# Kernel tuning notes

Measured on AMD Instinct MI355X. Metric: run time of the kernel, lower is better.

Reference implementation:

```python
import jax, jax.numpy as jnp
import numpy as np

B = 64          # graphs in batch
NPG = 9         # nodes per graph (max_atoms = NUM_ATOMS = 9)
N = B * NPG     # total nodes = 576
H = 128         # node_dim == hid_dim
SPEC_LEN = 1801
SPEC_COMP = 100
BOND = 3
ASL = BOND * 9 * 9  # action_space_length = 243


def _linear_init(key, fan_in, fan_out):
    # torch.nn.Linear default init: U(-1/sqrt(fan_in), 1/sqrt(fan_in)); stored as [in, out]
    kw, kb = jax.random.split(key)
    bound = 1.0 / np.sqrt(fan_in)
    W = jax.random.uniform(kw, (fan_in, fan_out), jnp.float32, -bound, bound)
    b = jax.random.uniform(kb, (fan_out,), jnp.float32, -bound, bound)
    return W, b


def setup_inputs() -> dict:
    key = jax.random.key(0)
    ks = jax.random.split(key, 10)
    node_features = jax.random.normal(ks[0], (N, H), jnp.float32)
    specs = jax.random.normal(ks[1], (B, 1, SPEC_LEN), jnp.float32)
    # len_vec[b, i] = 1 iff node i belongs to graph b (contiguous 9-node blocks)
    gid = np.repeat(np.arange(B), NPG)
    len_vec = jnp.asarray((gid[None, :] == np.arange(B)[:, None]).astype(np.float32))
    mask = jnp.zeros((B, ASL), jnp.float32)  # additive action mask (0 = allowed)
    indexmask = jax.random.randint(ks[2], (B, ASL), 0, ASL, dtype=jnp.int32)
    W1, b1 = _linear_init(ks[3], SPEC_LEN, SPEC_LEN // 2)
    W2, b2 = _linear_init(ks[4], SPEC_LEN // 2, SPEC_COMP)
    Wv1, bv1 = _linear_init(ks[5], H + SPEC_COMP, H // 2)
    Wv2, bv2 = _linear_init(ks[6], H // 2, 1)
    Wa2, ba2 = _linear_init(ks[7], 2 * H + SPEC_COMP, H)
    Wf, bf = _linear_init(ks[8], H, BOND)
    return {"node_features": node_features, "specs": specs, "len_vec": len_vec,
            "mask": mask, "indexmask": indexmask,
            "W1": W1, "b1": b1, "W2": W2, "b2": b2,
            "Wv1": Wv1, "bv1": bv1, "Wv2": Wv2, "bv2": bv2,
            "Wa2": Wa2, "ba2": ba2, "Wf": Wf, "bf": bf}


def reference(node_features, specs, len_vec, mask, indexmask,
              W1, b1, W2, b2, Wv1, bv1, Wv2, bv2, Wa2, ba2, Wf, bf):
    relu = jax.nn.relu
    n_total, hdim = node_features.shape
    bsz = specs.shape[0]
    npg = n_total // bsz

    # --- spectrum compression: [B,1801] -> [B,100] ---
    s = relu(specs[:, 0, :] @ W1 + b1)
    s = relu(s @ W2 + b2)

    # --- value head: SumPooling readout + spec -> scalar per graph ---
    readout = node_features.reshape(bsz, npg, hdim).sum(axis=1)
    v = relu(jnp.concatenate([readout, s], axis=-1) @ Wv1 + bv1) @ Wv2 + bv2  # [B,1]

    # --- pairwise action features ---
    # original: apf[i,j] = relu(cat(nf[i], nf[j], canvas[i,j])) then Linear(action_2).
    # relu is elementwise and Linear splits over the concat, so factorize:
    #   apf @ Wa2 = relu(nf)[i] @ Wa2[:H]  +  relu(nf)[j] @ Wa2[H:2H]  +  relu(canvas)[i,j] @ Wa2[2H:]
    # canvas is the block-diagonal scatter of s (s >= 0 so relu(canvas) = canvas).
    gid = jnp.arange(n_total) // npg
    same = gid[:, None] == gid[None, :]          # block-diagonal [N,N]
    nf_r = relu(node_features)
    Ai = nf_r @ Wa2[:hdim]                        # [N,H] per-row (Y2) term
    Bj = nf_r @ Wa2[hdim:2 * hdim]                # [N,H] per-col (X2) term
    D = s @ Wa2[2 * hdim:]                        # [B,H] spec-canvas term
    h = relu(Ai[:, None, :] + Bj[None, :, :]
             + jnp.where(same[:, :, None], D[gid][:, None, :], 0.0) + ba2)  # [N,N,H]

    len_matrix = (len_vec.T @ len_vec)[:, :, None]  # block-diagonal pair mask [N,N,1]
    saf = (h @ Wf + bf) * len_matrix                # [N,N,BOND]

    # --- per-graph action assembly (replaces nonzero()+pad+index_select loop) ---
    # with npg nodes per graph the nonzeros of saf are exactly the diagonal
    # npg x npg blocks, flattened (i, j, bond)-major, npg*npg*BOND == ASL.
    rows = jnp.arange(bsz)[:, None] * npg + jnp.arange(npg)[None, :]   # [B,npg]
    fp = saf[rows[:, :, None], rows[:, None, :], :].reshape(bsz, npg * npg * saf.shape[-1])
    gathered = jnp.take_along_axis(fp, indexmask.astype(jnp.int32), axis=1)
    return jax.nn.softmax(gathered + mask, axis=1), v
```

## Files before the change

### kernel.cpp

```cpp
#include <hip/hip_runtime.h>
#include <math.h>

#define BATCH 64
#define NPG 9
#define N_NODES 576
#define HD 128
#define SPEC_LEN 1801
#define S1DIM 900
#define SCOMP 100
#define ASL 243
#define NT 15
#define KC 17
#define KCH 106
#define KPAD 112
#define KT 1856

__global__ __launch_bounds__(256) void k_prep(const float* __restrict__ specs,
                                              const float* __restrict__ nf,
                                              const float* __restrict__ Wa2,
                                              float* __restrict__ sT,
                                              float* __restrict__ zbase,
                                              float* __restrict__ AB) {
    int bb = blockIdx.x, tid = threadIdx.x;
    if (bb < 29) {
        __shared__ float t[64 * 65];
        int k0 = bb * 64;
        int kk = tid & 63, mq = tid >> 6;
#pragma unroll
        for (int p = 0; p < 16; ++p) {
            int m = p * 4 + mq;
            int k = k0 + kk;
            float v = (k < SPEC_LEN) ? specs[(size_t)m * SPEC_LEN + k] : 0.0f;
            t[kk * 65 + m] = v;
        }
        __syncthreads();
#pragma unroll
        for (int p = 0; p < 16; ++p) {
            int o = p * 256 + tid;
            sT[(size_t)k0 * 64 + o] = t[(o >> 6) * 65 + (o & 63)];
        }
    } else if (bb < 92) {
        int idx = (bb - 29) * 1024 + tid * 4;
        if (idx < BATCH * S1DIM + BATCH * SCOMP)
            *(float4*)(zbase + idx) = make_float4(0.f, 0.f, 0.f, 0.f);
    } else {
        __shared__ float snf[4 * HD];
        int ib = (bb - 92) * 4;
        snf[tid]       = fmaxf(nf[(size_t)ib * HD + tid], 0.0f);
        snf[256 + tid] = fmaxf(nf[(size_t)ib * HD + 256 + tid], 0.0f);
        __syncthreads();
        int c = tid;
        const float* __restrict__ wp = (c < HD) ? (Wa2 + c) : (Wa2 + HD * HD + (c - HD));
        float a0 = 0.f, a1 = 0.f, a2 = 0.f, a3 = 0.f;
#pragma unroll 16
        for (int k = 0; k < HD; ++k) {
            float w = wp[(size_t)k * HD];
            a0 = fmaf(snf[k], w, a0);
            a1 = fmaf(snf[HD + k], w, a1);
            a2 = fmaf(snf[2 * HD + k], w, a2);
            a3 = fmaf(snf[3 * HD + k], w, a3);
        }
        AB[(size_t)(ib + 0) * 256 + c] = a0;
        AB[(size_t)(ib + 1) * 256 + c] = a1;
        AB[(size_t)(ib + 2) * 256 + c] = a2;
        AB[(size_t)(ib + 3) * 256 + c] = a3;
    }
}

__global__ __launch_bounds__(256) void k_gemm1(const float* __restrict__ sT,
                                               const float* __restrict__ W1,
                                               float* __restrict__ s1pre) {
    __shared__ float w1t[KPAD][64];
    int bb = blockIdx.x, tid = threadIdx.x;
    int nt = bb % NT, kc = bb / NT;
    int n0 = nt * 64;
    int kb = kc * KCH;
    int klen = min(KCH, SPEC_LEN - kb);
    int lane = tid & 63;
    int m0 = __builtin_amdgcn_readfirstlane(tid >> 6) * 16;

#pragma unroll 7
    for (int e = tid; e < KPAD * 64; e += 256) {
        int kl = e >> 6, nn = e & 63;
        float v = 0.0f;
        if (kl < klen && (n0 + nn) < S1DIM)
            v = W1[(size_t)(kb + kl) * S1DIM + n0 + nn];
        w1t[kl][nn] = v;
    }
    __syncthreads();

    float acc[16];
#pragma unroll
    for (int i = 0; i < 16; ++i) acc[i] = 0.0f;

    const float* __restrict__ sp = sT + (size_t)kb * 64 + m0;
#pragma unroll 4
    for (int kk = 0; kk < KPAD; ++kk) {
        float w = w1t[kk][lane];
        const float* __restrict__ sa = sp + kk * 64;
#pragma unroll
        for (int i = 0; i < 16; ++i)
            acc[i] = fmaf(sa[i], w, acc[i]);
    }

    int n = n0 + lane;
    if (n < S1DIM) {
#pragma unroll
        for (int i = 0; i < 16; ++i)
            atomicAdd(&s1pre[(size_t)(m0 + i) * S1DIM + n], acc[i]);
    }
}

__global__ __launch_bounds__(128) void k_gemm2(const float* __restrict__ s1pre,
                                               const float* __restrict__ b1,
                                               const float* __restrict__ W2,
                                               float* __restrict__ s1c) {
    __shared__ float sld[SCOMP];
    int bb = blockIdx.x, tid = threadIdx.x;
    int m = bb / 9;
    int kb = (bb % 9) * 100;
    if (tid < 100)
        sld[tid] = fmaxf(s1pre[(size_t)m * S1DIM + kb + tid] + b1[kb + tid], 0.0f);
    __syncthreads();
    if (tid < SCOMP) {
        float a = 0.0f;
#pragma unroll 10
        for (int kl = 0; kl < 100; ++kl)
            a = fmaf(sld[kl], W2[(size_t)(kb + kl) * SCOMP + tid], a);
        atomicAdd(&s1c[(size_t)m * SCOMP + tid], a);
    }
}

__global__ __launch_bounds__(256) void k_head(const float* __restrict__ s1c,
                                              const float* __restrict__ b2,
                                              const float* __restrict__ Wa2,
                                              const float* __restrict__ nf,
                                              const float* __restrict__ Wv1,
                                              const float* __restrict__ bv1,
                                              const float* __restrict__ Wv2,
                                              const float* __restrict__ bv2,
                                              const float* __restrict__ ba2,
                                              const float* __restrict__ Wf,
                                              const float* __restrict__ bfb,
                                              const int* __restrict__ indexmask,
                                              const float* __restrict__ mask,
                                              const float* __restrict__ AB,
                                              float* __restrict__ out,
                                              float* __restrict__ vout) {
    int m = blockIdx.x, tid = threadIdx.x;
    __shared__ __align__(16) float sAi[NPG * 132];
    __shared__ __align__(16) float sBj[NPG * 132];
    __shared__ __align__(16) float sWfT[3 * 132];
    __shared__ __align__(16) float srow[SCOMP];
    __shared__ __align__(16) float ro[HD];
    __shared__ __align__(16) float sC[HD];
    __shared__ float fp[ASL];
    __shared__ float red[8];

    for (int e = tid; e < NPG * 256; e += 256) {
        int i = e >> 8, c = e & 255;
        float v = AB[(size_t)(m * NPG + i) * 256 + c];
        if (c < HD) sAi[i * 132 + c] = v;
        else        sBj[i * 132 + (c - HD)] = v;
    }
    for (int e = tid; e < 3 * HD; e += 256)
        sWfT[(e % 3) * 132 + (e / 3)] = Wf[e];
    if (tid < SCOMP)
        srow[tid] = fmaxf(s1c[(size_t)m * SCOMP + tid] + b2[tid], 0.0f);
    if (tid >= 128) {
        int h = tid - 128;
        float a = 0.0f;
#pragma unroll
        for (int i = 0; i < NPG; ++i) a += nf[(size_t)(m * NPG + i) * HD + h];
        ro[h] = a;
    }
    __syncthreads();

    if (tid < HD) {
        float a = 0.0f;
#pragma unroll 10
        for (int k = 0; k < SCOMP; ++k)
            a = fmaf(srow[k], Wa2[(size_t)(2 * HD + k) * HD + tid], a);
        sC[tid] = a + ba2[tid];
    } else if (tid < 192) {
        int t = tid - 128;
        float a = bv1[t];
#pragma unroll 8
        for (int k = 0; k < HD; ++k) a = fmaf(ro[k], Wv1[(size_t)k * 64 + t], a);
#pragma unroll 10
        for (int k = 0; k < SCOMP; ++k) a = fmaf(srow[k], Wv1[(size_t)(HD + k) * 64 + t], a);
        a = fmaxf(a, 0.0f);
        float p = a * Wv2[t];
#pragma unroll
        for (int off = 32; off; off >>= 1) p += __shfl_down(p, off, 64);
        if (tid == 128) vout[m] = p + bv2[0];
    }
    __syncthreads();

    for (int e = tid; e < NPG * HD; e += 256)
        sAi[(e >> 7) * 132 + (e & 127)] += sC[e & 127];
    __syncthreads();

    if (tid < ASL) {
        int i = tid / 27;
        int j = (tid / 3) % 9;
        int bo = tid % 3;
        float a = bfb[bo];
        const float* pa = sAi + i * 132;
        const float* pb = sBj + j * 132;
        const float* pw = sWfT + bo * 132;
#pragma unroll 8
        for (int h = 0; h < HD; h += 4) {
            const float4 A = *(const float4*)&pa[h];
            const float4 Bv = *(const float4*)&pb[h];
            const float4 W = *(const float4*)&pw[h];
            a = fmaf(fmaxf(A.x + Bv.x, 0.f), W.x, a);
            a = fmaf(fmaxf(A.y + Bv.y, 0.f), W.y, a);
            a = fmaf(fmaxf(A.z + Bv.z, 0.f), W.z, a);
            a = fmaf(fmaxf(A.w + Bv.w, 0.f), W.w, a);
        }
        fp[tid] = a;
    }
    __syncthreads();

    float g = -INFINITY;
    if (tid < ASL) g = fp[indexmask[(size_t)m * ASL + tid]] + mask[(size_t)m * ASL + tid];
    float mx = g;
#pragma unroll
    for (int off = 32; off; off >>= 1) mx = fmaxf(mx, __shfl_down(mx, off, 64));
    if ((tid & 63) == 0) red[tid >> 6] = mx;
    __syncthreads();
    mx = fmaxf(fmaxf(red[0], red[1]), fmaxf(red[2], red[3]));
    float e = (tid < ASL) ? __expf(g - mx) : 0.0f;
    float sm = e;
#pragma unroll
    for (int off = 32; off; off >>= 1) sm += __shfl_down(sm, off, 64);
    if ((tid & 63) == 0) red[4 + (tid >> 6)] = sm;
    __syncthreads();
    sm = red[4] + red[5] + red[6] + red[7];
    if (tid < ASL) out[(size_t)m * ASL + tid] = e / sm;
}

extern "C" void kernel_launch(void* const* d_in, const int* in_sizes, int n_in,
                              void* d_out, int out_size, void* d_ws, size_t ws_size,
                              hipStream_t stream) {
    (void)in_sizes; (void)n_in; (void)out_size; (void)ws_size;
    const float* nf    = (const float*)d_in[0];
    const float* specs = (const float*)d_in[1];
    const float* mask  = (const float*)d_in[3];
    const int*   idxm  = (const int*)d_in[4];
    const float* W1  = (const float*)d_in[5];
    const float* b1  = (const float*)d_in[6];
    const float* W2  = (const float*)d_in[7];
    const float* b2  = (const float*)d_in[8];
    const float* Wv1 = (const float*)d_in[9];
    const float* bv1 = (const float*)d_in[10];
    const float* Wv2 = (const float*)d_in[11];
    const float* bv2 = (const float*)d_in[12];
    const float* Wa2 = (const float*)d_in[13];
    const float* ba2 = (const float*)d_in[14];
    const float* Wf  = (const float*)d_in[15];
    const float* bfv = (const float*)d_in[16];
    float* out = (float*)d_out;
    float* ws  = (float*)d_ws;

    float* sT    = ws;
    float* s1pre = sT + KT * 64;
    float* s1c   = s1pre + BATCH * S1DIM;
    float* AB    = s1c + BATCH * SCOMP;

    k_prep<<<dim3(92 + 144), dim3(256), 0, stream>>>(specs, nf, Wa2, sT, s1pre, AB);
    k_gemm1<<<dim3(NT * KC), dim3(256), 0, stream>>>(sT, W1, s1pre);
    k_gemm2<<<dim3(BATCH * 9), dim3(128), 0, stream>>>(s1pre, b1, W2, s1c);
    k_head<<<dim3(BATCH), dim3(256), 0, stream>>>(s1c, b2, Wa2, nf,
                                                  Wv1, bv1, Wv2, bv2, ba2, Wf, bfv,
                                                  idxm, mask, AB, out, out + BATCH * ASL);
}
```

Before: 137.4 us.

## Collapse four kernels into two with split-K partials instead of atomics

Folds the spec transpose into the first GEMM, which now loads specs directly into shared memory and uses a 4x4 register-tiled outer product. Split-K results are written as per-chunk partial buffers instead of atomics, so the zero-init pass goes away. The second GEMM moves into the head kernel: each graph block reduces the 17 partials, applies bias and ReLU, and computes its 100-wide compression in place. This removes two launches and the atomic traffic, at the cost of a larger partial buffer and serial GEMM2 work inside only 64 blocks.

```diff
diff --git a/kernel.cpp b/kernel.cpp
--- a/kernel.cpp
+++ b/kernel.cpp
@@ -13,39 +13,75 @@
 #define KC 17
 #define KCH 106
 #define KPAD 112
-#define KT 1856
-
-__global__ __launch_bounds__(256) void k_prep(const float* __restrict__ specs,
-                                              const float* __restrict__ nf,
-                                              const float* __restrict__ Wa2,
-                                              float* __restrict__ sT,
-                                              float* __restrict__ zbase,
-                                              float* __restrict__ AB) {
+
+__global__ __launch_bounds__(256) void k1(const float* __restrict__ specs,
+                                          const float* __restrict__ W1,
+                                          const float* __restrict__ nf,
+                                          const float* __restrict__ Wa2,
+                                          float* __restrict__ P,
+                                          float* __restrict__ AB) {
     int bb = blockIdx.x, tid = threadIdx.x;
-    if (bb < 29) {
-        __shared__ float t[64 * 65];
-        int k0 = bb * 64;
-        int kk = tid & 63, mq = tid >> 6;
-#pragma unroll
-        for (int p = 0; p < 16; ++p) {
-            int m = p * 4 + mq;
-            int k = k0 + kk;
-            float v = (k < SPEC_LEN) ? specs[(size_t)m * SPEC_LEN + k] : 0.0f;
-            t[kk * 65 + m] = v;
+    if (bb < NT * KC) {
+        __shared__ __align__(16) float sA[KPAD * 68];
+        __shared__ __align__(16) float sB[KPAD * 64];
+        int nt = bb % NT, kc = bb / NT;
+        int n0 = nt * 64, kb = kc * KCH;
+        int klen = min(KCH, SPEC_LEN - kb);
+
+#pragma unroll
+        for (int p = 0; p < 28; ++p) {
+            int e = p * 256 + tid;
+            int m = e / KPAD;
+            int k = e - m * KPAD;
+            float v = (k < klen) ? specs[(size_t)m * SPEC_LEN + kb + k] : 0.0f;
+            sA[k * 68 + m] = v;
+        }
+#pragma unroll
+        for (int p = 0; p < 7; ++p) {
+            int e = p * 256 + tid;
+            int kl = e >> 4, nq = (e & 15) * 4;
+            float4 v = make_float4(0.f, 0.f, 0.f, 0.f);
+            if (kl < klen && (n0 + nq) < S1DIM)
+                v = *(const float4*)&W1[(size_t)(kb + kl) * S1DIM + n0 + nq];
+            *(float4*)&sB[kl * 64 + nq] = v;
         }
         __syncthreads();
-#pragma unroll
-        for (int p = 0; p < 16; ++p) {
-            int o = p * 256 + tid;
-            sT[(size_t)k0 * 64 + o] = t[(o >> 6) * 65 + (o & 63)];
-        }
-    } else if (bb < 92) {
-        int idx = (bb - 29) * 1024 + tid * 4;
-        if (idx < BATCH * S1DIM + BATCH * SCOMP)
-            *(float4*)(zbase + idx) = make_float4(0.f, 0.f, 0.f, 0.f);
+
+        int tn = (tid & 15) * 4;
+        int tm = (tid >> 4) * 4;
+        float acc[4][4] = {};
+#pragma unroll 4
+        for (int k = 0; k < KPAD; ++k) {
+            const float4 a = *(const float4*)&sA[k * 68 + tm];
+            const float4 b = *(const float4*)&sB[k * 64 + tn];
+            acc[0][0] = fmaf(a.x, b.x, acc[0][0]);
+            acc[0][1] = fmaf(a.x, b.y, acc[0][1]);
+            acc[0][2] = fmaf(a.x, b.z, acc[0][2]);
+            acc[0][3] = fmaf(a.x, b.w, acc[0][3]);
+            acc[1][0] = fmaf(a.y, b.x, acc[1][0]);
+            acc[1][1] = fmaf(a.y, b.y, acc[1][1]);
+            acc[1][2] = fmaf(a.y, b.z, acc[1][2]);
+            acc[1][3] = fmaf(a.y, b.w, acc[1][3]);
+            acc[2][0] = fmaf(a.z, b.x, acc[2][0]);
+            acc[2][1] = fmaf(a.z, b.y, acc[2][1]);
+            acc[2][2] = fmaf(a.z, b.z, acc[2][2]);
+            acc[2][3] = fmaf(a.z, b.w, acc[2][3]);
+            acc[3][0] = fmaf(a.w, b.x, acc[3][0]);
+            acc[3][1] = fmaf(a.w, b.y, acc[3][1]);
+            acc[3][2] = fmaf(a.w, b.z, acc[3][2]);
+            acc[3][3] = fmaf(a.w, b.w, acc[3][3]);
+        }
+
+        if (n0 + tn < S1DIM) {
+#pragma unroll
+            for (int i = 0; i < 4; ++i) {
+                float4 o = make_float4(acc[i][0], acc[i][1], acc[i][2], acc[i][3]);
+                *(float4*)&P[((size_t)(kc * 64 + tm + i)) * S1DIM + n0 + tn] = o;
+            }
+        }
     } else {
         __shared__ float snf[4 * HD];
-        int ib = (bb - 92) * 4;
+        int ib = (bb - NT * KC) * 4;
         snf[tid]       = fmaxf(nf[(size_t)ib * HD + tid], 0.0f);
         snf[256 + tid] = fmaxf(nf[(size_t)ib * HD + 256 + tid], 0.0f);
         __syncthreads();
@@ -67,96 +103,43 @@
     }
 }
 
-__global__ __launch_bounds__(256) void k_gemm1(const float* __restrict__ sT,
-                                               const float* __restrict__ W1,
-                                               float* __restrict__ s1pre) {
-    __shared__ float w1t[KPAD][64];
-    int bb = blockIdx.x, tid = threadIdx.x;
-    int nt = bb % NT, kc = bb / NT;
-    int n0 = nt * 64;
-    int kb = kc * KCH;
-    int klen = min(KCH, SPEC_LEN - kb);
-    int lane = tid & 63;
-    int m0 = __builtin_amdgcn_readfirstlane(tid >> 6) * 16;
-
-#pragma unroll 7
-    for (int e = tid; e < KPAD * 64; e += 256) {
-        int kl = e >> 6, nn = e & 63;
-        float v = 0.0f;
-        if (kl < klen && (n0 + nn) < S1DIM)
-            v = W1[(size_t)(kb + kl) * S1DIM + n0 + nn];
-        w1t[kl][nn] = v;
-    }
-    __syncthreads();
-
-    float acc[16];
-#pragma unroll
-    for (int i = 0; i < 16; ++i) acc[i] = 0.0f;
-
-    const float* __restrict__ sp = sT + (size_t)kb * 64 + m0;
-#pragma unroll 4
-    for (int kk = 0; kk < KPAD; ++kk) {
-        float w = w1t[kk][lane];
-        const float* __restrict__ sa = sp + kk * 64;
-#pragma unroll
-        for (int i = 0; i < 16; ++i)
-            acc[i] = fmaf(sa[i], w, acc[i]);
-    }
-
-    int n = n0 + lane;
-    if (n < S1DIM) {
-#pragma unroll
-        for (int i = 0; i < 16; ++i)
-            atomicAdd(&s1pre[(size_t)(m0 + i) * S1DIM + n], acc[i]);
-    }
-}
-
-__global__ __launch_bounds__(128) void k_gemm2(const float* __restrict__ s1pre,
-                                               const float* __restrict__ b1,
-                                               const float* __restrict__ W2,
-                                               float* __restrict__ s1c) {
-    __shared__ float sld[SCOMP];
-    int bb = blockIdx.x, tid = threadIdx.x;
-    int m = bb / 9;
-    int kb = (bb % 9) * 100;
-    if (tid < 100)
-        sld[tid] = fmaxf(s1pre[(size_t)m * S1DIM + kb + tid] + b1[kb + tid], 0.0f);
-    __syncthreads();
-    if (tid < SCOMP) {
-        float a = 0.0f;
-#pragma unroll 10
-        for (int kl = 0; kl < 100; ++kl)
-            a = fmaf(sld[kl], W2[(size_t)(kb + kl) * SCOMP + tid], a);
-        atomicAdd(&s1c[(size_t)m * SCOMP + tid], a);
-    }
-}
-
-__global__ __launch_bounds__(256) void k_head(const float* __restrict__ s1c,
-                                              const float* __restrict__ b2,
-                                              const float* __restrict__ Wa2,
-                                              const float* __restrict__ nf,
-                                              const float* __restrict__ Wv1,
-                                              const float* __restrict__ bv1,
-                                              const float* __restrict__ Wv2,
-                                              const float* __restrict__ bv2,
-                                              const float* __restrict__ ba2,
-                                              const float* __restrict__ Wf,
-                                              const float* __restrict__ bfb,
-                                              const int* __restrict__ indexmask,
-                                              const float* __restrict__ mask,
-                                              const float* __restrict__ AB,
-                                              float* __restrict__ out,
-                                              float* __restrict__ vout) {
+__global__ __launch_bounds__(256) void k2(const float* __restrict__ P,
+                                          const float* __restrict__ b1,
+                                          const float* __restrict__ W2,
+                                          const float* __restrict__ b2,
+                                          const float* __restrict__ Wa2,
+                                          const float* __restrict__ nf,
+                                          const float* __restrict__ Wv1,
+                                          const float* __restrict__ bv1,
+                                          const float* __restrict__ Wv2,
+                                          const float* __restrict__ bv2,
+                                          const float* __restrict__ ba2,
+                                          const float* __restrict__ Wf,
+                                          const float* __restrict__ bfb,
+                                          const int* __restrict__ indexmask,
+                                          const float* __restrict__ mask,
+                                          const float* __restrict__ AB,
+                                          float* __restrict__ out,
+                                          float* __restrict__ vout) {
     int m = blockIdx.x, tid = threadIdx.x;
+    __shared__ __align__(16) float s1row[S1DIM];
     __shared__ __align__(16) float sAi[NPG * 132];
     __shared__ __align__(16) float sBj[NPG * 132];
     __shared__ __align__(16) float sWfT[3 * 132];
     __shared__ __align__(16) float srow[SCOMP];
     __shared__ __align__(16) float ro[HD];
     __shared__ __align__(16) float sC[HD];
+    __shared__ float part[200];
     __shared__ float fp[ASL];
     __shared__ float red[8];
 
+    for (int n = tid; n < S1DIM; n += 256) {
+        float a = b1[n];
+#pragma unroll
+        for (int kc = 0; kc < KC; ++kc)
+            a += P[((size_t)kc * 64 + m) * S1DIM + n];
+        s1row[n] = fmaxf(a, 0.0f);
+    }
     for (int e = tid; e < NPG * 256; e += 256) {
         int i = e >> 8, c = e & 255;
         float v = AB[(size_t)(m * NPG + i) * 256 + c];
@@ -165,8 +148,6 @@
     }
     for (int e = tid; e < 3 * HD; e += 256)
         sWfT[(e % 3) * 132 + (e / 3)] = Wf[e];
-    if (tid < SCOMP)
-        srow[tid] = fmaxf(s1c[(size_t)m * SCOMP + tid] + b2[tid], 0.0f);
     if (tid >= 128) {
         int h = tid - 128;
         float a = 0.0f;
@@ -174,6 +155,19 @@
         for (int i = 0; i < NPG; ++i) a += nf[(size_t)(m * NPG + i) * HD + h];
         ro[h] = a;
     }
+    __syncthreads();
+
+    if (tid < 200) {
+        int c = tid % 100;
+        int kb = (tid / 100) * 450;
+        float a = 0.0f;
+#pragma unroll 10
+        for (int kl = 0; kl < 450; ++kl)
+            a = fmaf(s1row[kb + kl], W2[(size_t)(kb + kl) * SCOMP + c], a);
+        part[tid] = a;
+    }
+    __syncthreads();
+    if (tid < SCOMP) srow[tid] = fmaxf(part[tid] + part[tid + 100] + b2[tid], 0.0f);
     __syncthreads();
 
     if (tid < HD) {
@@ -197,10 +191,6 @@
     }
     __syncthreads();
 
-    for (int e = tid; e < NPG * HD; e += 256)
-        sAi[(e >> 7) * 132 + (e & 127)] += sC[e & 127];
-    __syncthreads();
-
     if (tid < ASL) {
         int i = tid / 27;
         int j = (tid / 3) % 9;
@@ -213,11 +203,12 @@
         for (int h = 0; h < HD; h += 4) {
             const float4 A = *(const float4*)&pa[h];
             const float4 Bv = *(const float4*)&pb[h];
+            const float4 C = *(const float4*)&sC[h];
             const float4 W = *(const float4*)&pw[h];
-            a = fmaf(fmaxf(A.x + Bv.x, 0.f), W.x, a);
-            a = fmaf(fmaxf(A.y + Bv.y, 0.f), W.y, a);
-            a = fmaf(fmaxf(A.z + Bv.z, 0.f), W.z, a);
-            a = fmaf(fmaxf(A.w + Bv.w, 0.f), W.w, a);
+            a = fmaf(fmaxf(A.x + Bv.x + C.x, 0.f), W.x, a);
+            a = fmaf(fmaxf(A.y + Bv.y + C.y, 0.f), W.y, a);
+            a = fmaf(fmaxf(A.z + Bv.z + C.z, 0.f), W.z, a);
+            a = fmaf(fmaxf(A.w + Bv.w + C.w, 0.f), W.w, a);
         }
         fp[tid] = a;
     }
@@ -264,15 +255,11 @@
     float* out = (float*)d_out;
     float* ws  = (float*)d_ws;
 
-    float* sT    = ws;
-    float* s1pre = sT + KT * 64;
-    float* s1c   = s1pre + BATCH * S1DIM;
-    float* AB    = s1c + BATCH * SCOMP;
-
-    k_prep<<<dim3(92 + 144), dim3(256), 0, stream>>>(specs, nf, Wa2, sT, s1pre, AB);
-    k_gemm1<<<dim3(NT * KC), dim3(256), 0, stream>>>(sT, W1, s1pre);
-    k_gemm2<<<dim3(BATCH * 9), dim3(128), 0, stream>>>(s1pre, b1, W2, s1c);
-    k_head<<<dim3(BATCH), dim3(256), 0, stream>>>(s1c, b2, Wa2, nf,
-                                                  Wv1, bv1, Wv2, bv2, ba2, Wf, bfv,
-                                                  idxm, mask, AB, out, out + BATCH * ASL);
+    float* P  = ws;
+    float* AB = P + (size_t)KC * 64 * S1DIM;
+
+    k1<<<dim3(NT * KC + N_NODES / 4), dim3(256), 0, stream>>>(specs, W1, nf, Wa2, P, AB);
+    k2<<<dim3(BATCH), dim3(256), 0, stream>>>(P, b1, W2, b2, Wa2, nf,
+                                              Wv1, bv1, Wv2, bv2, ba2, Wf, bfv,
+                                              idxm, mask, AB, out, out + BATCH * ASL);
 }
```

Result: no change. 138.4 us (+0.7%).
